# Kernel optimization log

Hardware: AMD Instinct MI355X
Metric: run time of the kernel (lower is better)

## Reference

```python
import jax, jax.numpy as jnp
import numpy as np

D_MODEL = 1024
N_HEADS = 16
HEAD_DIM = D_MODEL // N_HEADS
SCALE = HEAD_DIM ** -0.5
MASK_FILL = -10000.0


def setup_inputs() -> dict:
    key = jax.random.key(0)
    ks = jax.random.split(key, 12)
    B, L, D = 2, 2048, D_MODEL
    inv = 1.0 / np.sqrt(D)
    inp = {
        "query": jax.random.normal(ks[0], (B, L, D), jnp.float32),
        "key": jax.random.normal(ks[1], (B, L, D), jnp.float32),
        "value": jax.random.normal(ks[2], (B, L, D), jnp.float32),
        "Wq": jax.random.normal(ks[3], (D, D), jnp.float32) * inv,
        "bq": jnp.zeros((D,), jnp.float32),
        "Wk": jax.random.normal(ks[4], (D, D), jnp.float32) * inv,
        "bk": jnp.zeros((D,), jnp.float32),
        "Wv": jax.random.normal(ks[5], (D, D), jnp.float32) * inv,
        "bv": jnp.zeros((D,), jnp.float32),
        "Wo": jax.random.normal(ks[6], (D, D), jnp.float32) * inv,
        "bo": jnp.zeros((D,), jnp.float32),
        "valid_mask": jax.random.randint(ks[7], (B, L), 0, 2).astype(jnp.bool_),
    }
    return inp


def reference(query, key, value, Wq, bq, Wk, bk, Wv, bv, Wo, bo, valid_mask):
    B, Lq, D = query.shape
    Lk = key.shape[1]
    H, HD = N_HEADS, HEAD_DIM
    # torch.nn.Linear: y = x @ W.T + b
    Q = (query @ Wq.T + bq).reshape(B, Lq, H, HD).transpose(0, 2, 1, 3)  # [B,H,Lq,HD]
    K = (key @ Wk.T + bk).reshape(B, Lk, H, HD).transpose(0, 2, 1, 3)    # [B,H,Lk,HD]
    V = (value @ Wv.T + bv).reshape(B, Lk, H, HD).transpose(0, 2, 1, 3)  # [B,H,Lk,HD]
    scores = jnp.einsum("bhqd,bhkd->bhqk", Q, K) * SCALE
    scores = jnp.where(valid_mask[:, None, None, :], scores, MASK_FILL)
    weights = jax.nn.softmax(scores, axis=-1)  # dropout is identity at inference
    out = jnp.einsum("bhqk,bhkd->bhqd", weights, V)
    out = out.transpose(0, 2, 1, 3).reshape(B, Lq, D)
    out = out @ Wo.T + bo
    # zero rows of fully-invalid batches
    gate = jnp.any(valid_mask, axis=1).astype(out.dtype)[:, None, None]
    return out * gate
```

## Files before the change

### kernel.cpp

```cpp
#include <hip/hip_runtime.h>
#include <hip/hip_bf16.h>

typedef __hip_bfloat16 bf16;
typedef __attribute__((ext_vector_type(8))) short s8v;
typedef __attribute__((ext_vector_type(4))) float f4v;

#define LOG2E 1.44269504088896340736f
#define CSCALE (0.125f * LOG2E)
#define MASK_B2 (-14426.950408889634f)
#define NEG_BIG (-30000.0f)

#define BB 2
#define LL 2048
#define DD 1024
#define HH 16
#define HD 64
#define MTOT 4096
#define PER_T 4194304

struct alignas(8) B4 { bf16 v[4]; };

__device__ __forceinline__ void async_cp16(const bf16* g, bf16* l) {
    __builtin_amdgcn_global_load_lds(
        (const __attribute__((address_space(1))) void*)g,
        (__attribute__((address_space(3))) void*)l, 16, 0, 0);
}

struct CvtArgs {
    const float* src[7];
    bf16* dst[7];
    int n[7];
};

__global__ __launch_bounds__(256) void cvt_kernel(CvtArgs args) {
    const int which = blockIdx.y;
    const float* __restrict__ src = args.src[which];
    bf16* __restrict__ dst = args.dst[which];
    const int n4 = args.n[which] >> 2;
    const int stride = gridDim.x * 256;
    for (int i = blockIdx.x * 256 + threadIdx.x; i < n4; i += stride) {
        const float4 f = ((const float4*)src)[i];
        B4 o;
        o.v[0] = __float2bfloat16(f.x);
        o.v[1] = __float2bfloat16(f.y);
        o.v[2] = __float2bfloat16(f.z);
        o.v[3] = __float2bfloat16(f.w);
        ((B4*)dst)[i] = o;
    }
}

struct QkvArgs {
    const bf16* A[3];
    const bf16* W[3];
    const float* bias[3];
    bf16* out[3];
};

template <int FUSED, int SWAP>
__device__ __forceinline__ void gemm_body(const bf16* __restrict__ A,
                                          const bf16* __restrict__ W,
                                          const float* __restrict__ bias,
                                          bf16* __restrict__ out_bf,
                                          float* __restrict__ out_f,
                                          float gatef, char* smem) {
    bf16* sA = (bf16*)smem;
    bf16* sB = (bf16*)(smem + 128 * 64 * 2);
    bf16* sE = (bf16*)smem;

    const int lane = threadIdx.x & 63;
    const int w = threadIdx.x >> 6;
    const int lr = lane & 15;
    const int quad = lane >> 4;
    const int wr = w >> 1, wc = w & 1;
    const int rbase = blockIdx.x * 128;
    const int cbase = blockIdx.y * 128;
    const int dma_r = lane >> 3;
    const int dma_cc = ((lane & 7) ^ dma_r) * 8;

    f4v acc[4][4] = {};
    for (int kt = 0; kt < DD / 64; kt++) {
        const int k0 = kt * 64;
        __syncthreads();
#pragma unroll
        for (int t = 0; t < 4; t++) {
            const int g = w * 4 + t;
            async_cp16(A + (size_t)(rbase + g * 8 + dma_r) * DD + k0 + dma_cc,
                       &sA[g * 512]);
            async_cp16(W + (size_t)(cbase + g * 8 + dma_r) * DD + k0 + dma_cc,
                       &sB[g * 512]);
        }
        __syncthreads();
#pragma unroll
        for (int s = 0; s < 2; s++) {
            s8v a[4], b[4];
#pragma unroll
            for (int i = 0; i < 4; i++) {
                const int row = wr * 64 + i * 16 + lr;
                a[i] = *(const s8v*)&sA[row * 64 + (((s * 4 + quad) ^ (row & 7)) * 8)];
            }
#pragma unroll
            for (int j = 0; j < 4; j++) {
                const int row = wc * 64 + j * 16 + lr;
                b[j] = *(const s8v*)&sB[row * 64 + (((s * 4 + quad) ^ (row & 7)) * 8)];
            }
#pragma unroll
            for (int i = 0; i < 4; i++)
#pragma unroll
                for (int j = 0; j < 4; j++)
                    acc[i][j] = SWAP
                        ? __builtin_amdgcn_mfma_f32_16x16x32_bf16(b[j], a[i], acc[i][j], 0, 0, 0)
                        : __builtin_amdgcn_mfma_f32_16x16x32_bf16(a[i], b[j], acc[i][j], 0, 0, 0);
        }
    }
    __syncthreads();

    if (FUSED == 0) {
#pragma unroll
        for (int j = 0; j < 4; j++) {
            const int n = cbase + wc * 64 + j * 16 + quad * 4;
            const f4v bv = *(const f4v*)&bias[n];
#pragma unroll
            for (int i = 0; i < 4; i++) {
                const int m = rbase + wr * 64 + i * 16 + lr;
                float4 o;
                o.x = (acc[i][j][0] + bv[0]) * gatef;
                o.y = (acc[i][j][1] + bv[1]) * gatef;
                o.z = (acc[i][j][2] + bv[2]) * gatef;
                o.w = (acc[i][j][3] + bv[3]) * gatef;
                *(float4*)&out_f[(size_t)m * DD + n] = o;
            }
        }
        return;
    }

    if (SWAP) {
#pragma unroll
        for (int j = 0; j < 4; j++) {
            const int n_loc = wc * 64 + j * 16 + quad * 4;
            const f4v bv = *(const f4v*)&bias[cbase + n_loc];
#pragma unroll
            for (int i = 0; i < 4; i++) {
                const int m_loc = wr * 64 + i * 16 + lr;
                B4 pk;
                pk.v[0] = __float2bfloat16(acc[i][j][0] + bv[0]);
                pk.v[1] = __float2bfloat16(acc[i][j][1] + bv[1]);
                pk.v[2] = __float2bfloat16(acc[i][j][2] + bv[2]);
                pk.v[3] = __float2bfloat16(acc[i][j][3] + bv[3]);
                *(B4*)&sE[m_loc * 136 + n_loc] = pk;
            }
        }
        __syncthreads();
        const int tid = threadIdx.x;
        const int mr_ = tid >> 4;
        const int n0 = (tid & 15) * 8;
#pragma unroll
        for (int ro = 0; ro < 8; ro++) {
            const int m_loc = ro * 16 + mr_;
            const s8v vv = *(const s8v*)&sE[m_loc * 136 + n0];
            const int m = rbase + m_loc;
            const int n = cbase + n0;
            const int b_ = m >> 11, l = m & (LL - 1);
            const int h = n >> 6, hd = n & 63;
            *(s8v*)&out_bf[(((size_t)(b_ * HH + h)) * LL + l) * HD + hd] = vv;
        }
    } else {
#pragma unroll
        for (int j = 0; j < 4; j++) {
            const int n_loc = wc * 64 + j * 16 + lr;
            const float bv = bias[cbase + n_loc];
#pragma unroll
            for (int i = 0; i < 4; i++) {
                const int m0 = wr * 64 + i * 16 + quad * 4;
                B4 pk;
                pk.v[0] = __float2bfloat16(acc[i][j][0] + bv);
                pk.v[1] = __float2bfloat16(acc[i][j][1] + bv);
                pk.v[2] = __float2bfloat16(acc[i][j][2] + bv);
                pk.v[3] = __float2bfloat16(acc[i][j][3] + bv);
                *(B4*)&sE[n_loc * 136 + m0] = pk;
            }
        }
        __syncthreads();
        const int tid = threadIdx.x;
#pragma unroll
        for (int ro = 0; ro < 8; ro++) {
            const int n_loc = ro * 16 + (tid >> 4);
            const int m0 = (tid & 15) * 8;
            const s8v vv = *(const s8v*)&sE[n_loc * 136 + m0];
            const int n = cbase + n_loc;
            const int m = rbase + m0;
            const int b_ = m >> 11, l = m & (LL - 1);
            const int h = n >> 6, hd = n & 63;
            *(s8v*)&out_bf[(((size_t)(b_ * HH + h)) * HD + hd) * LL + l] = vv;
        }
    }
}

template <int FUSED>
__global__ __launch_bounds__(256) void gemm128(QkvArgs qa,
                                               const bf16* __restrict__ Ao,
                                               const bf16* __restrict__ Wo_,
                                               const float* __restrict__ bo_,
                                               float* __restrict__ out_f,
                                               const int* __restrict__ mask) {
    __shared__ __align__(16) char smem[128 * 136 * 2];
    __shared__ int sgate;

    float gatef = 1.0f;
    if (!FUSED) {
        if (threadIdx.x == 0) sgate = 0;
        __syncthreads();
        const int b_ = (int)(blockIdx.x * 128) >> 11;
        int any = 0;
        for (int i = threadIdx.x; i < LL; i += 256) any |= mask[b_ * LL + i];
        if (any) sgate = 1;
        __syncthreads();
        gatef = sgate ? 1.0f : 0.0f;
    }

    if (FUSED) {
        const int which = blockIdx.z;
        if (which != 2)
            gemm_body<1, 1>(qa.A[which], qa.W[which], qa.bias[which],
                            qa.out[which], nullptr, 1.0f, smem);
        else
            gemm_body<1, 0>(qa.A[2], qa.W[2], qa.bias[2],
                            qa.out[2], nullptr, 1.0f, smem);
    } else {
        gemm_body<0, 1>(Ao, Wo_, bo_, nullptr, out_f, gatef, smem);
    }
}

__global__ __launch_bounds__(512) void attn_kernel(const bf16* __restrict__ Q,
                                                   const bf16* __restrict__ K,
                                                   const bf16* __restrict__ Vt,
                                                   const int* __restrict__ mask,
                                                   bf16* __restrict__ Aout) {
    __shared__ bf16 sK[2][64 * 64];
    __shared__ bf16 sV[2][64 * 64];
    __shared__ float sBias[LL];

    const int lane = threadIdx.x & 63;
    const int w = threadIdx.x >> 6;
    const int lr = lane & 15;
    const int quad = lane >> 4;

    const int bid = blockIdx.x;
    const int qb = bid & 15;
    const int h = (bid >> 4) & 15;
    const int b = bid >> 8;

    const size_t head_off = ((size_t)(b * HH + h)) * LL * HD;
    const bf16* Qh = Q + head_off;
    const bf16* Kh = K + head_off;
    const bf16* Vh = Vt + head_off;
    const int q0 = qb * 128 + w * 16;

    const int dma_r = lane >> 3;
    const int dma_cv = ((lane & 7) ^ dma_r) * 8;
    const int dma_ck = ((lane & 7) ^ ((dma_r & 3) | ((w & 1) << 2))) * 8;

    {
        const int* mb = mask + b * LL;
        for (int i = threadIdx.x; i < LL; i += 512)
            sBias[i] = mb[i] ? 0.0f : MASK_B2;
        async_cp16(Kh + (size_t)(w * 8 + dma_r) * HD + dma_ck, &sK[0][w * 512]);
        async_cp16(Vh + (size_t)(w * 8 + dma_r) * LL + dma_cv, &sV[0][w * 512]);
    }
    __syncthreads();

    const s8v aq0 = *(const s8v*)(Qh + (size_t)(q0 + lr) * HD + quad * 8);
    const s8v aq1 = *(const s8v*)(Qh + (size_t)(q0 + lr) * HD + 32 + quad * 8);

    f4v O[4] = {};
    float mrun = NEG_BIG, lrun = 0.0f;

    const int swk = (lr & 3) | (((lr >> 2) & 1) << 2);
    const int swv = lr & 7;
    const int krow0 = 8 * (lr >> 2) + (lr & 3);

    for (int kt = 0; kt < LL / 64; kt++) {
        const int kbase = kt * 64;
        const bf16* kb = &sK[kt & 1][0];
        const bf16* vb = &sV[kt & 1][0];

        if (kt < LL / 64 - 1) {
            const int nb = (kt + 1) & 1;
            async_cp16(Kh + (size_t)(kbase + 64 + w * 8 + dma_r) * HD + dma_ck,
                       &sK[nb][w * 512]);
            async_cp16(Vh + (size_t)(w * 8 + dma_r) * LL + kbase + 64 + dma_cv,
                       &sV[nb][w * 512]);
        }

        f4v T[4];
#pragma unroll
        for (int j = 0; j < 4; j++) {
            const int row = krow0 + 32 * (j >> 1) + 4 * (j & 1);
            const s8v kb0 = *(const s8v*)&kb[row * 64 + ((quad ^ swk) * 8)];
            const s8v kb1 = *(const s8v*)&kb[row * 64 + (((quad + 4) ^ swk) * 8)];
            f4v t = {};
            t = __builtin_amdgcn_mfma_f32_16x16x32_bf16(kb0, aq0, t, 0, 0, 0);
            T[j] = __builtin_amdgcn_mfma_f32_16x16x32_bf16(kb1, aq1, t, 0, 0, 0);
        }

        s8v v0[4], v1[4];
#pragma unroll
        for (int dt = 0; dt < 4; dt++) {
            const int vrow = dt * 16 + lr;
            v0[dt] = *(const s8v*)&vb[vrow * 64 + ((quad ^ swv) * 8)];
            v1[dt] = *(const s8v*)&vb[vrow * 64 + (((quad + 4) ^ swv) * 8)];
        }

        float mloc = NEG_BIG;
#pragma unroll
        for (int j = 0; j < 4; j++) {
            const f4v bj = *(const f4v*)&sBias[kbase + 32 * (j >> 1) + 8 * quad + 4 * (j & 1)];
#pragma unroll
            for (int r = 0; r < 4; r++) {
                T[j][r] = T[j][r] * CSCALE + bj[r];
                mloc = fmaxf(mloc, T[j][r]);
            }
        }
        mloc = fmaxf(mloc, __shfl_xor(mloc, 16));
        mloc = fmaxf(mloc, __shfl_xor(mloc, 32));

        if (__any(mloc > mrun)) {
            const float mnew = fmaxf(mrun, mloc);
            const float alphaq = exp2f(mrun - mnew);
            mrun = mnew;
            lrun *= alphaq;
#pragma unroll
            for (int dt = 0; dt < 4; dt++)
#pragma unroll
                for (int r = 0; r < 4; r++) O[dt][r] *= alphaq;
        }

        float ls = 0.0f;
#pragma unroll
        for (int j = 0; j < 4; j++)
#pragma unroll
            for (int r = 0; r < 4; r++) {
                const float e = exp2f(T[j][r] - mrun);
                T[j][r] = e;
                ls += e;
            }
        ls += __shfl_xor(ls, 16);
        ls += __shfl_xor(ls, 32);
        lrun += ls;

        union { s8v v; bf16 e[8]; } p0, p1;
#pragma unroll
        for (int r = 0; r < 4; r++) {
            p0.e[r]     = __float2bfloat16(T[0][r]);
            p0.e[r + 4] = __float2bfloat16(T[1][r]);
            p1.e[r]     = __float2bfloat16(T[2][r]);
            p1.e[r + 4] = __float2bfloat16(T[3][r]);
        }

#pragma unroll
        for (int dt = 0; dt < 4; dt++) {
            O[dt] = __builtin_amdgcn_mfma_f32_16x16x32_bf16(v0[dt], p0.v, O[dt], 0, 0, 0);
            O[dt] = __builtin_amdgcn_mfma_f32_16x16x32_bf16(v1[dt], p1.v, O[dt], 0, 0, 0);
        }

        __syncthreads();
    }

    const float linv = 1.0f / lrun;
#pragma unroll
    for (int dt = 0; dt < 4; dt++) {
        B4 o;
#pragma unroll
        for (int r = 0; r < 4; r++) o.v[r] = __float2bfloat16(O[dt][r] * linv);
        *(B4*)&Aout[((size_t)(b * LL + q0 + lr)) * DD + h * HD + dt * 16 + quad * 4] = o;
    }
}

extern "C" void kernel_launch(void* const* d_in, const int* in_sizes, int n_in,
                              void* d_out, int out_size, void* d_ws, size_t ws_size,
                              hipStream_t stream) {
    const float* query = (const float*)d_in[0];
    const float* key   = (const float*)d_in[1];
    const float* value = (const float*)d_in[2];
    const float* Wq = (const float*)d_in[3];
    const float* bq = (const float*)d_in[4];
    const float* Wk = (const float*)d_in[5];
    const float* bk = (const float*)d_in[6];
    const float* Wv = (const float*)d_in[7];
    const float* bv = (const float*)d_in[8];
    const float* Wo = (const float*)d_in[9];
    const float* bo = (const float*)d_in[10];
    const int* mask = (const int*)d_in[11];

    bf16* base = (bf16*)d_ws;
    bf16* qx = base;
    bf16* kx = qx + PER_T;
    bf16* vx = kx + PER_T;
    bf16* wq = vx + PER_T;
    bf16* wk = wq + DD * DD;
    bf16* wv = wk + DD * DD;
    bf16* wo = wv + DD * DD;
    bf16* Qs = wo + DD * DD;
    bf16* Ks = Qs + PER_T;
    bf16* Vst = Ks + PER_T;
    bf16* aws = Vst + PER_T;

    CvtArgs ca;
    ca.src[0] = query; ca.dst[0] = qx; ca.n[0] = PER_T;
    ca.src[1] = key;   ca.dst[1] = kx; ca.n[1] = PER_T;
    ca.src[2] = value; ca.dst[2] = vx; ca.n[2] = PER_T;
    ca.src[3] = Wq;    ca.dst[3] = wq; ca.n[3] = DD * DD;
    ca.src[4] = Wk;    ca.dst[4] = wk; ca.n[4] = DD * DD;
    ca.src[5] = Wv;    ca.dst[5] = wv; ca.n[5] = DD * DD;
    ca.src[6] = Wo;    ca.dst[6] = wo; ca.n[6] = DD * DD;
    cvt_kernel<<<dim3(1024, 7), 256, 0, stream>>>(ca);

    QkvArgs qa;
    qa.A[0] = qx; qa.W[0] = wq; qa.bias[0] = bq; qa.out[0] = Qs;
    qa.A[1] = kx; qa.W[1] = wk; qa.bias[1] = bk; qa.out[1] = Ks;
    qa.A[2] = vx; qa.W[2] = wv; qa.bias[2] = bv; qa.out[2] = Vst;

    gemm128<1><<<dim3(MTOT / 128, DD / 128, 3), 256, 0, stream>>>(
        qa, nullptr, nullptr, nullptr, nullptr, nullptr);

    attn_kernel<<<BB * HH * (LL / 128), 512, 0, stream>>>(Qs, Ks, Vst, mask, aws);

    QkvArgs dummy{};
    gemm128<0><<<dim3(MTOT / 128, DD / 128, 1), 256, 0, stream>>>(
        dummy, aws, wo, bo, (float*)d_out, mask);
}
```

Baseline: 254.6 us.

## Process two query tiles per wave in attention, halve block threads

The attention kernel now uses 4 waves of 256 threads instead of 8, and each wave handles 32 query rows (two 16-row chunks), so each K/V fragment read from LDS feeds two MFMA chains. This cuts LDS read traffic per FLOP and gives more independent MFMAs to hide latency. Each thread now issues two async copies each for K and V, and s_setprio hints are added around the MFMA sections. The cost is higher register pressure from doubled O, T and softmax state, and fewer waves per block, which could lower occupancy.

New measurement: 269.3 us. 1.06x slower.

```diff
diff --git a/kernel.cpp b/kernel.cpp
--- a/kernel.cpp
+++ b/kernel.cpp
@@ -230,7 +230,7 @@
     }
 }
 
-__global__ __launch_bounds__(512) void attn_kernel(const bf16* __restrict__ Q,
+__global__ __launch_bounds__(256) void attn_kernel(const bf16* __restrict__ Q,
                                                    const bf16* __restrict__ K,
                                                    const bf16* __restrict__ Vt,
                                                    const int* __restrict__ mask,
@@ -253,26 +253,35 @@
     const bf16* Qh = Q + head_off;
     const bf16* Kh = K + head_off;
     const bf16* Vh = Vt + head_off;
-    const int q0 = qb * 128 + w * 16;
+    const int q0 = qb * 128 + w * 32;
 
     const int dma_r = lane >> 3;
     const int dma_cv = ((lane & 7) ^ dma_r) * 8;
-    const int dma_ck = ((lane & 7) ^ ((dma_r & 3) | ((w & 1) << 2))) * 8;
+    const int dma_ck0 = ((lane & 7) ^ (dma_r & 3)) * 8;
+    const int dma_ck1 = ((lane & 7) ^ ((dma_r & 3) | 4)) * 8;
 
     {
         const int* mb = mask + b * LL;
-        for (int i = threadIdx.x; i < LL; i += 512)
+        for (int i = threadIdx.x; i < LL; i += 256)
             sBias[i] = mb[i] ? 0.0f : MASK_B2;
-        async_cp16(Kh + (size_t)(w * 8 + dma_r) * HD + dma_ck, &sK[0][w * 512]);
-        async_cp16(Vh + (size_t)(w * 8 + dma_r) * LL + dma_cv, &sV[0][w * 512]);
+        const int g0 = w * 2, g1 = w * 2 + 1;
+        async_cp16(Kh + (size_t)(g0 * 8 + dma_r) * HD + dma_ck0, &sK[0][g0 * 512]);
+        async_cp16(Kh + (size_t)(g1 * 8 + dma_r) * HD + dma_ck1, &sK[0][g1 * 512]);
+        async_cp16(Vh + (size_t)(g0 * 8 + dma_r) * LL + dma_cv, &sV[0][g0 * 512]);
+        async_cp16(Vh + (size_t)(g1 * 8 + dma_r) * LL + dma_cv, &sV[0][g1 * 512]);
     }
     __syncthreads();
 
-    const s8v aq0 = *(const s8v*)(Qh + (size_t)(q0 + lr) * HD + quad * 8);
-    const s8v aq1 = *(const s8v*)(Qh + (size_t)(q0 + lr) * HD + 32 + quad * 8);
-
-    f4v O[4] = {};
-    float mrun = NEG_BIG, lrun = 0.0f;
+    s8v aq[2][2];
+#pragma unroll
+    for (int qc = 0; qc < 2; qc++) {
+        aq[qc][0] = *(const s8v*)(Qh + (size_t)(q0 + qc * 16 + lr) * HD + quad * 8);
+        aq[qc][1] = *(const s8v*)(Qh + (size_t)(q0 + qc * 16 + lr) * HD + 32 + quad * 8);
+    }
+
+    f4v O[2][4] = {};
+    float mrun[2] = {NEG_BIG, NEG_BIG};
+    float lrun[2] = {0.0f, 0.0f};
 
     const int swk = (lr & 3) | (((lr >> 2) & 1) << 2);
     const int swv = lr & 7;
@@ -285,22 +294,32 @@
 
         if (kt < LL / 64 - 1) {
             const int nb = (kt + 1) & 1;
-            async_cp16(Kh + (size_t)(kbase + 64 + w * 8 + dma_r) * HD + dma_ck,
-                       &sK[nb][w * 512]);
-            async_cp16(Vh + (size_t)(w * 8 + dma_r) * LL + kbase + 64 + dma_cv,
-                       &sV[nb][w * 512]);
-        }
-
-        f4v T[4];
+            const int g0 = w * 2, g1 = w * 2 + 1;
+            async_cp16(Kh + (size_t)(kbase + 64 + g0 * 8 + dma_r) * HD + dma_ck0,
+                       &sK[nb][g0 * 512]);
+            async_cp16(Kh + (size_t)(kbase + 64 + g1 * 8 + dma_r) * HD + dma_ck1,
+                       &sK[nb][g1 * 512]);
+            async_cp16(Vh + (size_t)(g0 * 8 + dma_r) * LL + kbase + 64 + dma_cv,
+                       &sV[nb][g0 * 512]);
+            async_cp16(Vh + (size_t)(g1 * 8 + dma_r) * LL + kbase + 64 + dma_cv,
+                       &sV[nb][g1 * 512]);
+        }
+
+        f4v T[2][4];
+        __builtin_amdgcn_s_setprio(1);
 #pragma unroll
         for (int j = 0; j < 4; j++) {
             const int row = krow0 + 32 * (j >> 1) + 4 * (j & 1);
             const s8v kb0 = *(const s8v*)&kb[row * 64 + ((quad ^ swk) * 8)];
             const s8v kb1 = *(const s8v*)&kb[row * 64 + (((quad + 4) ^ swk) * 8)];
-            f4v t = {};
-            t = __builtin_amdgcn_mfma_f32_16x16x32_bf16(kb0, aq0, t, 0, 0, 0);
-            T[j] = __builtin_amdgcn_mfma_f32_16x16x32_bf16(kb1, aq1, t, 0, 0, 0);
-        }
+#pragma unroll
+            for (int qc = 0; qc < 2; qc++) {
+                f4v t = {};
+                t = __builtin_amdgcn_mfma_f32_16x16x32_bf16(kb0, aq[qc][0], t, 0, 0, 0);
+                T[qc][j] = __builtin_amdgcn_mfma_f32_16x16x32_bf16(kb1, aq[qc][1], t, 0, 0, 0);
+            }
+        }
+        __builtin_amdgcn_s_setprio(0);
 
         s8v v0[4], v1[4];
 #pragma unroll
@@ -310,68 +329,81 @@
             v1[dt] = *(const s8v*)&vb[vrow * 64 + (((quad + 4) ^ swv) * 8)];
         }
 
-        float mloc = NEG_BIG;
-#pragma unroll
-        for (int j = 0; j < 4; j++) {
-            const f4v bj = *(const f4v*)&sBias[kbase + 32 * (j >> 1) + 8 * quad + 4 * (j & 1)];
+        f4v bj[4];
+#pragma unroll
+        for (int j = 0; j < 4; j++)
+            bj[j] = *(const f4v*)&sBias[kbase + 32 * (j >> 1) + 8 * quad + 4 * (j & 1)];
+
+        union { s8v v; bf16 e[8]; } p0[2], p1[2];
+#pragma unroll
+        for (int qc = 0; qc < 2; qc++) {
+            float mloc = NEG_BIG;
+#pragma unroll
+            for (int j = 0; j < 4; j++)
+#pragma unroll
+                for (int r = 0; r < 4; r++) {
+                    T[qc][j][r] = T[qc][j][r] * CSCALE + bj[j][r];
+                    mloc = fmaxf(mloc, T[qc][j][r]);
+                }
+            mloc = fmaxf(mloc, __shfl_xor(mloc, 16));
+            mloc = fmaxf(mloc, __shfl_xor(mloc, 32));
+
+            if (__any(mloc > mrun[qc])) {
+                const float mnew = fmaxf(mrun[qc], mloc);
+                const float alphaq = exp2f(mrun[qc] - mnew);
+                mrun[qc] = mnew;
+                lrun[qc] *= alphaq;
+#pragma unroll
+                for (int dt = 0; dt < 4; dt++)
+#pragma unroll
+                    for (int r = 0; r < 4; r++) O[qc][dt][r] *= alphaq;
+            }
+
+            float ls = 0.0f;
+#pragma unroll
+            for (int j = 0; j < 4; j++)
+#pragma unroll
+                for (int r = 0; r < 4; r++) {
+                    const float e = exp2f(T[qc][j][r] - mrun[qc]);
+                    T[qc][j][r] = e;
+                    ls += e;
+                }
+            ls += __shfl_xor(ls, 16);
+            ls += __shfl_xor(ls, 32);
+            lrun[qc] += ls;
+
 #pragma unroll
             for (int r = 0; r < 4; r++) {
-                T[j][r] = T[j][r] * CSCALE + bj[r];
-                mloc = fmaxf(mloc, T[j][r]);
-            }
-        }
-        mloc = fmaxf(mloc, __shfl_xor(mloc, 16));
-        mloc = fmaxf(mloc, __shfl_xor(mloc, 32));
-
-        if (__any(mloc > mrun)) {
-            const float mnew = fmaxf(mrun, mloc);
-            const float alphaq = exp2f(mrun - mnew);
-            mrun = mnew;
-            lrun *= alphaq;
-#pragma unroll
-            for (int dt = 0; dt < 4; dt++)
-#pragma unroll
-                for (int r = 0; r < 4; r++) O[dt][r] *= alphaq;
-        }
-
-        float ls = 0.0f;
-#pragma unroll
-        for (int j = 0; j < 4; j++)
-#pragma unroll
-            for (int r = 0; r < 4; r++) {
-                const float e = exp2f(T[j][r] - mrun);
-                T[j][r] = e;
-                ls += e;
-            }
-        ls += __shfl_xor(ls, 16);
-        ls += __shfl_xor(ls, 32);
-        lrun += ls;
-
-        union { s8v v; bf16 e[8]; } p0, p1;
-#pragma unroll
-        for (int r = 0; r < 4; r++) {
-            p0.e[r]     = __float2bfloat16(T[0][r]);
-            p0.e[r + 4] = __float2bfloat16(T[1][r]);
-            p1.e[r]     = __float2bfloat16(T[2][r]);
-            p1.e[r + 4] = __float2bfloat16(T[3][r]);
-        }
-
+                p0[qc].e[r]     = __float2bfloat16(T[qc][0][r]);
+                p0[qc].e[r + 4] = __float2bfloat16(T[qc][1][r]);
+                p1[qc].e[r]     = __float2bfloat16(T[qc][2][r]);
+                p1[qc].e[r + 4] = __float2bfloat16(T[qc][3][r]);
+            }
+        }
+
+        __builtin_amdgcn_s_setprio(1);
+#pragma unroll
+        for (int qc = 0; qc < 2; qc++)
+#pragma unroll
+            for (int dt = 0; dt < 4; dt++) {
+                O[qc][dt] = __builtin_amdgcn_mfma_f32_16x16x32_bf16(v0[dt], p0[qc].v, O[qc][dt], 0, 0, 0);
+                O[qc][dt] = __builtin_amdgcn_mfma_f32_16x16x32_bf16(v1[dt], p1[qc].v, O[qc][dt], 0, 0, 0);
+            }
+        __builtin_amdgcn_s_setprio(0);
+
+        __syncthreads();
+    }
+
+#pragma unroll
+    for (int qc = 0; qc < 2; qc++) {
+        const float linv = 1.0f / lrun[qc];
 #pragma unroll
         for (int dt = 0; dt < 4; dt++) {
-            O[dt] = __builtin_amdgcn_mfma_f32_16x16x32_bf16(v0[dt], p0.v, O[dt], 0, 0, 0);
-            O[dt] = __builtin_amdgcn_mfma_f32_16x16x32_bf16(v1[dt], p1.v, O[dt], 0, 0, 0);
-        }
-
-        __syncthreads();
-    }
-
-    const float linv = 1.0f / lrun;
-#pragma unroll
-    for (int dt = 0; dt < 4; dt++) {
-        B4 o;
-#pragma unroll
-        for (int r = 0; r < 4; r++) o.v[r] = __float2bfloat16(O[dt][r] * linv);
-        *(B4*)&Aout[((size_t)(b * LL + q0 + lr)) * DD + h * HD + dt * 16 + quad * 4] = o;
+            B4 o;
+#pragma unroll
+            for (int r = 0; r < 4; r++) o.v[r] = __float2bfloat16(O[qc][dt][r] * linv);
+            *(B4*)&Aout[((size_t)(b * LL + q0 + qc * 16 + lr)) * DD + h * HD + dt * 16 + quad * 4] = o;
+        }
     }
 }
 
@@ -422,7 +454,7 @@
     gemm128<1><<<dim3(MTOT / 128, DD / 128, 3), 256, 0, stream>>>(
         qa, nullptr, nullptr, nullptr, nullptr, nullptr);
 
-    attn_kernel<<<BB * HH * (LL / 128), 512, 0, stream>>>(Qs, Ks, Vst, mask, aws);
+    attn_kernel<<<BB * HH * (LL / 128), 256, 0, stream>>>(Qs, Ks, Vst, mask, aws);
 
     QkvArgs dummy{};
     gemm128<0><<<dim3(MTOT / 128, DD / 128, 1), 256, 0, stream>>>(
```
